# Optimization experiments

Hardware: AMD Instinct MI355X
Metric: run time of the kernel (lower is better)

Reference implementation:

```python
import jax, jax.numpy as jnp
import numpy as np

BETA_MIN = 0.1
BETA_MAX = 20.0
T_MIN = 1e-4
T_MAX = 1.0
N_ITER = 256
B, D, K = 8192, 32, 64


def setup_inputs() -> dict:
    key = jax.random.key(0)
    k1, k2, k3, k4, k5 = jax.random.split(key, 5)
    return {
        "x_init": jax.random.normal(k1, (B, D), jnp.float32),
        "centers": jax.random.normal(k2, (K, D), jnp.float32),
        # stds kept away from 0 so the t->0 mixture variances stay well conditioned
        "stds": jax.random.uniform(k3, (K, D), jnp.float32, minval=0.2, maxval=1.0),
        "weights": jax.random.uniform(k4, (K,), jnp.float32, minval=0.1, maxval=1.0),
        # Brownian increments for every Euler-Maruyama step (pre-drawn for determinism)
        "noise": jax.random.normal(k5, (N_ITER - 1, B, D), jnp.float32),
    }


def _beta(t):
    # linear beta schedule
    return BETA_MIN + (BETA_MAX - BETA_MIN) * t


def _Beta(t):
    # integral of beta
    return BETA_MIN * t + 0.5 * (BETA_MAX - BETA_MIN) * t * t


def reference(x_init, centers, stds, weights, noise):
    log_w = jnp.log(weights)  # [K]
    times = jnp.linspace(T_MIN, T_MAX, N_ITER)[::-1]  # reversed schedule

    def grad_log_prob(x, t):
        # exact Gaussian-mixture score of the VP-diffused density at time t
        eB = jnp.exp(-_Beta(t))
        m = jnp.sqrt(eB) * centers                    # [K, D] diffused means
        v = eB * stds * stds + (1.0 - eB)             # [K, D] diffused variances
        diff = x[:, None, :] - m[None, :, :]          # [B, K, D]
        # faithful to the original (including the ndim/2 * sum(log) normalization term)
        logc = (-0.5 * jnp.sum(diff * diff / v, axis=-1)
                - (0.5 * D) * jnp.sum(jnp.log(2.0 * np.pi * v), axis=-1)
                + log_w)                              # [B, K]
        r = jax.nn.softmax(logc, axis=1)              # responsibilities [B, K]
        return -jnp.einsum('bk,bkd->bd', r, diff / v) # grad_x log p_t(x)

    def step(x, inp):
        t, t_next, z = inp
        dt = t_next - t                               # negative (reverse time)
        bt = _beta(t)
        score = grad_log_prob(x, t)
        # reverse VP-SDE drift: f - g^2 * score = -0.5*beta*x - beta*score
        drift = -0.5 * bt * x - bt * score
        x = x + drift * dt + jnp.sqrt(bt) * z * jnp.sqrt(jnp.abs(dt))
        return x, None

    x, _ = jax.lax.scan(step, x_init, (times[:-1], times[1:], noise))
    return x
```

## Files before the change

### kernel.cpp

```cpp
#include <hip/hip_runtime.h>
#include <math.h>


namespace {

constexpr int BD   = 8192;
constexpr int DIMN = 32;
constexpr int KM   = 64;
constexpr int NST  = 255;
constexpr float TMINc = 1e-4f, TMAXc = 1.0f;
constexpr float BMIN = 0.1f,  BMAX = 20.0f;
constexpr float L2E = 1.4426950408889634f;
constexpr float LN2 = 0.6931471805599453f;

template <int CTRL>
__device__ __forceinline__ float dpp_addf(float v) {
  int o = __builtin_amdgcn_update_dpp(0, __float_as_int(v), CTRL, 0xf, 0xf, true);
  return v + __int_as_float(o);
}
__device__ __forceinline__ float dred8(float v) {
  v = dpp_addf<0xB1>(v);
  v = dpp_addf<0x4E>(v);
  v = dpp_addf<0x141>(v);
  return v;
}

__global__ __launch_bounds__(256, 2) void sbm_kernel(
    const float* __restrict__ xin,
    const float* __restrict__ cen_g,
    const float* __restrict__ std_g,
    const float* __restrict__ w_g,
    const float* __restrict__ noi,
    float* __restrict__ out)
{
  __shared__ __align__(16) float s_iv[2][KM][DIMN];
  __shared__ __align__(16) float s_a [2][KM][DIMN];
  __shared__ __align__(16) float s_c [2][KM];
  __shared__ __align__(16) float4 s_n [2][4][2][64];
  __shared__ float2 s_ml[2][4][2][8];

  const int tid  = threadIdx.x;
  const int w    = tid >> 6;
  const int lane = tid & 63;
  const int dc   = lane & 7;
  const int slot = lane >> 3;
  const int d0   = dc * 4;
  const int k0   = w * 16;
  const int b0   = blockIdx.x * 16 + slot;
  const int b1   = b0 + 8;

  const int gk = tid >> 2;
  const int gd = (tid & 3) * 8;

  float cen[8], s2[8];
#pragma unroll
  for (int i = 0; i < 8; ++i) {
    cen[i] = cen_g[gk * DIMN + gd + i];
    float s = std_g[gk * DIMN + gd + i];
    s2[i] = s * s;
  }
  const float lw2 = __builtin_amdgcn_logf(w_g[gk]);

  float x0[4], x1[4];
  {
    const float4 a = *reinterpret_cast<const float4*>(xin + b0 * DIMN + d0);
    const float4 b = *reinterpret_cast<const float4*>(xin + b1 * DIMN + d0);
    x0[0]=a.x; x0[1]=a.y; x0[2]=a.z; x0[3]=a.w;
    x1[0]=b.x; x1[1]=b.y; x1[2]=b.z; x1[3]=b.w;
  }

  auto gen = [&](int buf, int jj) {
    const float t  = fmaf((float)(255 - jj) * (1.0f / 255.0f), (TMAXc - TMINc), TMINc);
    const float Bt = fmaf(0.5f * (BMAX - BMIN), t * t, BMIN * t);
    const float eB  = __builtin_amdgcn_exp2f(-Bt * L2E);
    const float om  = 1.0f - eB;
    const float smB = __builtin_amdgcn_sqrtf(eB);
    float cq = 0.0f, c2 = 0.0f;
    float ivv[8], av[8];
#pragma unroll
    for (int i = 0; i < 8; ++i) {
      const float v  = fmaf(eB, s2[i], om);
      const float iv = L2E * __builtin_amdgcn_rcpf(v);
      const float m  = smB * cen[i];
      const float A  = m * iv;
      ivv[i] = iv; av[i] = A;
      cq = fmaf(m, A, cq);
      c2 += __builtin_amdgcn_logf(v);
    }
    *reinterpret_cast<float4*>(&s_iv[buf][gk][gd])     = make_float4(ivv[0], ivv[1], ivv[2], ivv[3]);
    *reinterpret_cast<float4*>(&s_iv[buf][gk][gd + 4]) = make_float4(ivv[4], ivv[5], ivv[6], ivv[7]);
    *reinterpret_cast<float4*>(&s_a [buf][gk][gd])     = make_float4(av[0], av[1], av[2], av[3]);
    *reinterpret_cast<float4*>(&s_a [buf][gk][gd + 4]) = make_float4(av[4], av[5], av[6], av[7]);
    float q1 = dpp_addf<0xB1>(cq); q1 = dpp_addf<0x4E>(q1);
    float q2 = dpp_addf<0xB1>(c2); q2 = dpp_addf<0x4E>(q2);
    if ((tid & 3) == 0)
      s_c[buf][gk] = fmaf(-16.0f, q2, fmaf(-0.5f, q1, lw2));
  };

  gen(0, 0);
  __syncthreads();

#pragma unroll 1
  for (int j = 0; j < NST; ++j) {
    const int buf = j & 1;

    const float4 z0 = *reinterpret_cast<const float4*>(
        noi + ((size_t)j * BD + b0) * (size_t)DIMN + d0);
    const float4 z1 = *reinterpret_cast<const float4*>(
        noi + ((size_t)j * BD + b1) * (size_t)DIMN + d0);

    if (j + 1 < NST) gen(buf ^ 1, j + 1);

    const float t  = fmaf((float)(255 - j) * (1.0f / 255.0f), (TMAXc - TMINc), TMINc);
    const float tn = fmaf((float)(254 - j) * (1.0f / 255.0f), (TMAXc - TMINc), TMINc);
    const float dt = tn - t;
    const float bt = fmaf(BMAX - BMIN, t, BMIN);

    float h0[4], h1[4];
#pragma unroll
    for (int i = 0; i < 4; ++i) { h0[i] = -0.5f * x0[i] * x0[i]; h1[i] = -0.5f * x1[i] * x1[i]; }

    float M0 = -__builtin_inff(), M1 = -__builtin_inff();
    float L0 = 0.0f, L1 = 0.0f;
    float SIV0[4] = {0,0,0,0}, SA0[4] = {0,0,0,0};
    float SIV1[4] = {0,0,0,0}, SA1[4] = {0,0,0,0};

#pragma unroll
    for (int c = 0; c < 2; ++c) {
      const int kc = k0 + c * 8;
      const float4 ccl = *reinterpret_cast<const float4*>(&s_c[buf][kc]);
      const float4 cch = *reinterpret_cast<const float4*>(&s_c[buf][kc + 4]);
      const float cc[8] = {ccl.x, ccl.y, ccl.z, ccl.w, cch.x, cch.y, cch.z, cch.w};

      float4 tiv[8], ta[8];
      float p0[8], p1[8];
      float cm0 = -__builtin_inff(), cm1 = -__builtin_inff();
#pragma unroll
      for (int kk = 0; kk < 8; ++kk) {
        tiv[kk] = *reinterpret_cast<const float4*>(&s_iv[buf][kc + kk][d0]);
        ta[kk]  = *reinterpret_cast<const float4*>(&s_a [buf][kc + kk][d0]);
        float pa = h0[0] * tiv[kk].x;
        pa = fmaf(x0[0], ta[kk].x, pa);
        pa = fmaf(h0[1], tiv[kk].y, pa);
        pa = fmaf(x0[1], ta[kk].y, pa);
        pa = fmaf(h0[2], tiv[kk].z, pa);
        pa = fmaf(x0[2], ta[kk].z, pa);
        pa = fmaf(h0[3], tiv[kk].w, pa);
        pa = fmaf(x0[3], ta[kk].w, pa);
        float pb = h1[0] * tiv[kk].x;
        pb = fmaf(x1[0], ta[kk].x, pb);
        pb = fmaf(h1[1], tiv[kk].y, pb);
        pb = fmaf(x1[1], ta[kk].y, pb);
        pb = fmaf(h1[2], tiv[kk].z, pb);
        pb = fmaf(x1[2], ta[kk].z, pb);
        pb = fmaf(h1[3], tiv[kk].w, pb);
        pb = fmaf(x1[3], ta[kk].w, pb);
        pa = dred8(pa) + cc[kk];
        pb = dred8(pb) + cc[kk];
        p0[kk] = pa; p1[kk] = pb;
        cm0 = fmaxf(cm0, pa); cm1 = fmaxf(cm1, pb);
      }
      const float nM0 = fmaxf(M0, cm0), nM1 = fmaxf(M1, cm1);
      const float al0 = __builtin_amdgcn_exp2f(M0 - nM0);
      const float al1 = __builtin_amdgcn_exp2f(M1 - nM1);
      M0 = nM0; M1 = nM1;
      L0 *= al0; L1 *= al1;
#pragma unroll
      for (int i = 0; i < 4; ++i) {
        SIV0[i] *= al0; SA0[i] *= al0;
        SIV1[i] *= al1; SA1[i] *= al1;
      }
#pragma unroll
      for (int kk = 0; kk < 8; ++kk) {
        const float e0 = __builtin_amdgcn_exp2f(p0[kk] - M0);
        const float e1 = __builtin_amdgcn_exp2f(p1[kk] - M1);
        L0 += e0; L1 += e1;
        SIV0[0] = fmaf(e0, tiv[kk].x, SIV0[0]);
        SIV0[1] = fmaf(e0, tiv[kk].y, SIV0[1]);
        SIV0[2] = fmaf(e0, tiv[kk].z, SIV0[2]);
        SIV0[3] = fmaf(e0, tiv[kk].w, SIV0[3]);
        SA0[0]  = fmaf(e0, ta[kk].x, SA0[0]);
        SA0[1]  = fmaf(e0, ta[kk].y, SA0[1]);
        SA0[2]  = fmaf(e0, ta[kk].z, SA0[2]);
        SA0[3]  = fmaf(e0, ta[kk].w, SA0[3]);
        SIV1[0] = fmaf(e1, tiv[kk].x, SIV1[0]);
        SIV1[1] = fmaf(e1, tiv[kk].y, SIV1[1]);
        SIV1[2] = fmaf(e1, tiv[kk].z, SIV1[2]);
        SIV1[3] = fmaf(e1, tiv[kk].w, SIV1[3]);
        SA1[0]  = fmaf(e1, ta[kk].x, SA1[0]);
        SA1[1]  = fmaf(e1, ta[kk].y, SA1[1]);
        SA1[2]  = fmaf(e1, ta[kk].z, SA1[2]);
        SA1[3]  = fmaf(e1, ta[kk].w, SA1[3]);
      }
    }

    const float4 n0 = make_float4(fmaf(-x0[0], SIV0[0], SA0[0]),
                                  fmaf(-x0[1], SIV0[1], SA0[1]),
                                  fmaf(-x0[2], SIV0[2], SA0[2]),
                                  fmaf(-x0[3], SIV0[3], SA0[3]));
    const float4 n1 = make_float4(fmaf(-x1[0], SIV1[0], SA1[0]),
                                  fmaf(-x1[1], SIV1[1], SA1[1]),
                                  fmaf(-x1[2], SIV1[2], SA1[2]),
                                  fmaf(-x1[3], SIV1[3], SA1[3]));
    s_n[buf][w][0][lane] = n0;
    s_n[buf][w][1][lane] = n1;
    if (dc == 0) {
      s_ml[buf][w][0][slot] = make_float2(M0, L0);
      s_ml[buf][w][1][slot] = make_float2(M1, L1);
    }
    __syncthreads();

    const float cA  = fmaf(-0.5f * bt, dt, 1.0f);
    const float cb0 = (-bt * dt) * LN2;
    const float sq  = __builtin_amdgcn_sqrtf(bt) * __builtin_amdgcn_sqrtf(-dt);
    const int w1 = w ^ 1, w2 = w ^ 2, w3 = w ^ 3;

    {
      const float2 mA = s_ml[buf][w1][0][slot];
      const float2 mB = s_ml[buf][w2][0][slot];
      const float2 mC = s_ml[buf][w3][0][slot];
      const float Gm = fmaxf(fmaxf(M0, mA.x), fmaxf(mB.x, mC.x));
      const float ss = __builtin_amdgcn_exp2f(M0 - Gm);
      const float sA = __builtin_amdgcn_exp2f(mA.x - Gm);
      const float sB = __builtin_amdgcn_exp2f(mB.x - Gm);
      const float sC = __builtin_amdgcn_exp2f(mC.x - Gm);
      float Lt = ss * L0;
      Lt = fmaf(sA, mA.y, Lt); Lt = fmaf(sB, mB.y, Lt); Lt = fmaf(sC, mC.y, Lt);
      const float4 nA = s_n[buf][w1][0][lane];
      const float4 nB = s_n[buf][w2][0][lane];
      const float4 nC = s_n[buf][w3][0][lane];
      float nu[4] = {ss * n0.x, ss * n0.y, ss * n0.z, ss * n0.w};
      nu[0] = fmaf(sA, nA.x, nu[0]); nu[1] = fmaf(sA, nA.y, nu[1]);
      nu[2] = fmaf(sA, nA.z, nu[2]); nu[3] = fmaf(sA, nA.w, nu[3]);
      nu[0] = fmaf(sB, nB.x, nu[0]); nu[1] = fmaf(sB, nB.y, nu[1]);
      nu[2] = fmaf(sB, nB.z, nu[2]); nu[3] = fmaf(sB, nB.w, nu[3]);
      nu[0] = fmaf(sC, nC.x, nu[0]); nu[1] = fmaf(sC, nC.y, nu[1]);
      nu[2] = fmaf(sC, nC.z, nu[2]); nu[3] = fmaf(sC, nC.w, nu[3]);
      const float cb2 = cb0 * __builtin_amdgcn_rcpf(Lt);
      const float zc[4] = {z0.x, z0.y, z0.z, z0.w};
#pragma unroll
      for (int i = 0; i < 4; ++i)
        x0[i] = fmaf(cb2, nu[i], fmaf(cA, x0[i], sq * zc[i]));
    }
    {
      const float2 mA = s_ml[buf][w1][1][slot];
      const float2 mB = s_ml[buf][w2][1][slot];
      const float2 mC = s_ml[buf][w3][1][slot];
      const float Gm = fmaxf(fmaxf(M1, mA.x), fmaxf(mB.x, mC.x));
      const float ss = __builtin_amdgcn_exp2f(M1 - Gm);
      const float sA = __builtin_amdgcn_exp2f(mA.x - Gm);
      const float sB = __builtin_amdgcn_exp2f(mB.x - Gm);
      const float sC = __builtin_amdgcn_exp2f(mC.x - Gm);
      float Lt = ss * L1;
      Lt = fmaf(sA, mA.y, Lt); Lt = fmaf(sB, mB.y, Lt); Lt = fmaf(sC, mC.y, Lt);
      const float4 nA = s_n[buf][w1][1][lane];
      const float4 nB = s_n[buf][w2][1][lane];
      const float4 nC = s_n[buf][w3][1][lane];
      float nu[4] = {ss * n1.x, ss * n1.y, ss * n1.z, ss * n1.w};
      nu[0] = fmaf(sA, nA.x, nu[0]); nu[1] = fmaf(sA, nA.y, nu[1]);
      nu[2] = fmaf(sA, nA.z, nu[2]); nu[3] = fmaf(sA, nA.w, nu[3]);
      nu[0] = fmaf(sB, nB.x, nu[0]); nu[1] = fmaf(sB, nB.y, nu[1]);
      nu[2] = fmaf(sB, nB.z, nu[2]); nu[3] = fmaf(sB, nB.w, nu[3]);
      nu[0] = fmaf(sC, nC.x, nu[0]); nu[1] = fmaf(sC, nC.y, nu[1]);
      nu[2] = fmaf(sC, nC.z, nu[2]); nu[3] = fmaf(sC, nC.w, nu[3]);
      const float cb2 = cb0 * __builtin_amdgcn_rcpf(Lt);
      const float zc[4] = {z1.x, z1.y, z1.z, z1.w};
#pragma unroll
      for (int i = 0; i < 4; ++i)
        x1[i] = fmaf(cb2, nu[i], fmaf(cA, x1[i], sq * zc[i]));
    }
  }

  if (w == 0) {
    *reinterpret_cast<float4*>(out + b0 * DIMN + d0) = make_float4(x0[0], x0[1], x0[2], x0[3]);
    *reinterpret_cast<float4*>(out + b1 * DIMN + d0) = make_float4(x1[0], x1[1], x1[2], x1[3]);
  }
}

}

extern "C" void kernel_launch(void* const* d_in, const int* in_sizes, int n_in,
                              void* d_out, int out_size, void* d_ws, size_t ws_size,
                              hipStream_t stream) {
  const float* x_init  = (const float*)d_in[0];
  const float* centers = (const float*)d_in[1];
  const float* stds    = (const float*)d_in[2];
  const float* weights = (const float*)d_in[3];
  const float* noise   = (const float*)d_in[4];
  float* out = (float*)d_out;

  sbm_kernel<<<dim3(512), dim3(256), 0, stream>>>(x_init, centers, stds, weights,
                                                  noise, out);
}
```

Before: 1.172 ms.

## Split mixture components across eight waves and merge via shared-memory x state

```diff
diff --git a/kernel.cpp b/kernel.cpp
--- a/kernel.cpp
+++ b/kernel.cpp
@@ -25,7 +25,7 @@
   return v;
 }
 
-__global__ __launch_bounds__(256, 2) void sbm_kernel(
+__global__ __launch_bounds__(512, 4) void sbm_kernel(
     const float* __restrict__ xin,
     const float* __restrict__ cen_g,
     const float* __restrict__ std_g,
@@ -33,11 +33,12 @@
     const float* __restrict__ noi,
     float* __restrict__ out)
 {
-  __shared__ __align__(16) float s_iv[2][KM][DIMN];
-  __shared__ __align__(16) float s_a [2][KM][DIMN];
-  __shared__ __align__(16) float s_c [2][KM];
-  __shared__ __align__(16) float4 s_n [2][4][2][64];
-  __shared__ float2 s_ml[2][4][2][8];
+  __shared__ __align__(16) float  s_iv[2][KM][DIMN];
+  __shared__ __align__(16) float  s_a [2][KM][DIMN];
+  __shared__ __align__(16) float  s_c [2][KM];
+  __shared__ __align__(16) float4 s_n [8][16][8];
+  __shared__ __align__(16) float2 s_ml[8][16];
+  __shared__ __align__(16) float  s_x [16][DIMN];
 
   const int tid  = threadIdx.x;
   const int w    = tid >> 6;
@@ -45,29 +46,22 @@
   const int dc   = lane & 7;
   const int slot = lane >> 3;
   const int d0   = dc * 4;
-  const int k0   = w * 16;
-  const int b0   = blockIdx.x * 16 + slot;
-  const int b1   = b0 + 8;
-
-  const int gk = tid >> 2;
-  const int gd = (tid & 3) * 8;
-
-  float cen[8], s2[8];
-#pragma unroll
-  for (int i = 0; i < 8; ++i) {
-    cen[i] = cen_g[gk * DIMN + gd + i];
-    float s = std_g[gk * DIMN + gd + i];
-    s2[i] = s * s;
+  const int k0   = w * 8;
+  const int bbase = blockIdx.x * 16;
+
+  const int gk = tid >> 3;
+  const int gd = (tid & 7) * 4;
+  float cen[4], s2[4];
+  {
+    const float4 c4 = *reinterpret_cast<const float4*>(cen_g + gk * DIMN + gd);
+    const float4 s4 = *reinterpret_cast<const float4*>(std_g + gk * DIMN + gd);
+    cen[0]=c4.x; cen[1]=c4.y; cen[2]=c4.z; cen[3]=c4.w;
+    s2[0]=s4.x*s4.x; s2[1]=s4.y*s4.y; s2[2]=s4.z*s4.z; s2[3]=s4.w*s4.w;
   }
   const float lw2 = __builtin_amdgcn_logf(w_g[gk]);
 
-  float x0[4], x1[4];
-  {
-    const float4 a = *reinterpret_cast<const float4*>(xin + b0 * DIMN + d0);
-    const float4 b = *reinterpret_cast<const float4*>(xin + b1 * DIMN + d0);
-    x0[0]=a.x; x0[1]=a.y; x0[2]=a.z; x0[3]=a.w;
-    x1[0]=b.x; x1[1]=b.y; x1[2]=b.z; x1[3]=b.w;
-  }
+  const int mb = (w << 1) + (lane >> 5);
+  const int md = lane & 31;
 
   auto gen = [&](int buf, int jj) {
     const float t  = fmaf((float)(255 - jj) * (1.0f / 255.0f), (TMAXc - TMINc), TMINc);
@@ -75,28 +69,28 @@
     const float eB  = __builtin_amdgcn_exp2f(-Bt * L2E);
     const float om  = 1.0f - eB;
     const float smB = __builtin_amdgcn_sqrtf(eB);
-    float cq = 0.0f, c2 = 0.0f;
-    float ivv[8], av[8];
-#pragma unroll
-    for (int i = 0; i < 8; ++i) {
+    float cq = 0.0f, pv = 1.0f;
+    float ivv[4], av[4];
+#pragma unroll
+    for (int i = 0; i < 4; ++i) {
       const float v  = fmaf(eB, s2[i], om);
       const float iv = L2E * __builtin_amdgcn_rcpf(v);
       const float m  = smB * cen[i];
       const float A  = m * iv;
       ivv[i] = iv; av[i] = A;
       cq = fmaf(m, A, cq);
-      c2 += __builtin_amdgcn_logf(v);
-    }
-    *reinterpret_cast<float4*>(&s_iv[buf][gk][gd])     = make_float4(ivv[0], ivv[1], ivv[2], ivv[3]);
-    *reinterpret_cast<float4*>(&s_iv[buf][gk][gd + 4]) = make_float4(ivv[4], ivv[5], ivv[6], ivv[7]);
-    *reinterpret_cast<float4*>(&s_a [buf][gk][gd])     = make_float4(av[0], av[1], av[2], av[3]);
-    *reinterpret_cast<float4*>(&s_a [buf][gk][gd + 4]) = make_float4(av[4], av[5], av[6], av[7]);
-    float q1 = dpp_addf<0xB1>(cq); q1 = dpp_addf<0x4E>(q1);
-    float q2 = dpp_addf<0xB1>(c2); q2 = dpp_addf<0x4E>(q2);
-    if ((tid & 3) == 0)
+      pv *= v;
+    }
+    *reinterpret_cast<float4*>(&s_iv[buf][gk][gd]) = make_float4(ivv[0], ivv[1], ivv[2], ivv[3]);
+    *reinterpret_cast<float4*>(&s_a [buf][gk][gd]) = make_float4(av[0], av[1], av[2], av[3]);
+    const float q1 = dred8(cq);
+    const float q2 = dred8(__builtin_amdgcn_logf(pv));
+    if ((tid & 7) == 0)
       s_c[buf][gk] = fmaf(-16.0f, q2, fmaf(-0.5f, q1, lw2));
   };
 
+  float x_m = xin[(size_t)(bbase + mb) * DIMN + md];
+  s_x[mb][md] = x_m;
   gen(0, 0);
   __syncthreads();
 
@@ -104,10 +98,15 @@
   for (int j = 0; j < NST; ++j) {
     const int buf = j & 1;
 
-    const float4 z0 = *reinterpret_cast<const float4*>(
-        noi + ((size_t)j * BD + b0) * (size_t)DIMN + d0);
-    const float4 z1 = *reinterpret_cast<const float4*>(
-        noi + ((size_t)j * BD + b1) * (size_t)DIMN + d0);
+    const float z_m = noi[((size_t)j * BD + (bbase + mb)) * (size_t)DIMN + md];
+
+    float x0[4], x1[4];
+    {
+      const float4 a = *reinterpret_cast<const float4*>(&s_x[slot][d0]);
+      const float4 b = *reinterpret_cast<const float4*>(&s_x[slot + 8][d0]);
+      x0[0]=a.x; x0[1]=a.y; x0[2]=a.z; x0[3]=a.w;
+      x1[0]=b.x; x1[1]=b.y; x1[2]=b.z; x1[3]=b.w;
+    }
 
     if (j + 1 < NST) gen(buf ^ 1, j + 1);
 
@@ -120,23 +119,22 @@
 #pragma unroll
     for (int i = 0; i < 4; ++i) { h0[i] = -0.5f * x0[i] * x0[i]; h1[i] = -0.5f * x1[i] * x1[i]; }
 
-    float M0 = -__builtin_inff(), M1 = -__builtin_inff();
+    float M0 = 0.0f, M1 = 0.0f;
     float L0 = 0.0f, L1 = 0.0f;
     float SIV0[4] = {0,0,0,0}, SA0[4] = {0,0,0,0};
     float SIV1[4] = {0,0,0,0}, SA1[4] = {0,0,0,0};
 
 #pragma unroll
-    for (int c = 0; c < 2; ++c) {
-      const int kc = k0 + c * 8;
-      const float4 ccl = *reinterpret_cast<const float4*>(&s_c[buf][kc]);
-      const float4 cch = *reinterpret_cast<const float4*>(&s_c[buf][kc + 4]);
-      const float cc[8] = {ccl.x, ccl.y, ccl.z, ccl.w, cch.x, cch.y, cch.z, cch.w};
-
-      float4 tiv[8], ta[8];
-      float p0[8], p1[8];
+    for (int sc = 0; sc < 2; ++sc) {
+      const int kc = k0 + sc * 4;
+      const float4 ccv = *reinterpret_cast<const float4*>(&s_c[buf][kc]);
+      const float cc[4] = {ccv.x, ccv.y, ccv.z, ccv.w};
+
+      float4 tiv[4], ta[4];
+      float p0[4], p1[4];
       float cm0 = -__builtin_inff(), cm1 = -__builtin_inff();
 #pragma unroll
-      for (int kk = 0; kk < 8; ++kk) {
+      for (int kk = 0; kk < 4; ++kk) {
         tiv[kk] = *reinterpret_cast<const float4*>(&s_iv[buf][kc + kk][d0]);
         ta[kk]  = *reinterpret_cast<const float4*>(&s_a [buf][kc + kk][d0]);
         float pa = h0[0] * tiv[kk].x;
@@ -160,18 +158,22 @@
         p0[kk] = pa; p1[kk] = pb;
         cm0 = fmaxf(cm0, pa); cm1 = fmaxf(cm1, pb);
       }
-      const float nM0 = fmaxf(M0, cm0), nM1 = fmaxf(M1, cm1);
-      const float al0 = __builtin_amdgcn_exp2f(M0 - nM0);
-      const float al1 = __builtin_amdgcn_exp2f(M1 - nM1);
-      M0 = nM0; M1 = nM1;
-      L0 *= al0; L1 *= al1;
-#pragma unroll
-      for (int i = 0; i < 4; ++i) {
-        SIV0[i] *= al0; SA0[i] *= al0;
-        SIV1[i] *= al1; SA1[i] *= al1;
-      }
-#pragma unroll
-      for (int kk = 0; kk < 8; ++kk) {
+      if (sc == 0) {
+        M0 = cm0; M1 = cm1;
+      } else {
+        const float nM0 = fmaxf(M0, cm0), nM1 = fmaxf(M1, cm1);
+        const float al0 = __builtin_amdgcn_exp2f(M0 - nM0);
+        const float al1 = __builtin_amdgcn_exp2f(M1 - nM1);
+        M0 = nM0; M1 = nM1;
+        L0 *= al0; L1 *= al1;
+#pragma unroll
+        for (int i = 0; i < 4; ++i) {
+          SIV0[i] *= al0; SA0[i] *= al0;
+          SIV1[i] *= al1; SA1[i] *= al1;
+        }
+      }
+#pragma unroll
+      for (int kk = 0; kk < 4; ++kk) {
         const float e0 = __builtin_amdgcn_exp2f(p0[kk] - M0);
         const float e1 = __builtin_amdgcn_exp2f(p1[kk] - M1);
         L0 += e0; L1 += e1;
@@ -194,86 +196,51 @@
       }
     }
 
-    const float4 n0 = make_float4(fmaf(-x0[0], SIV0[0], SA0[0]),
-                                  fmaf(-x0[1], SIV0[1], SA0[1]),
-                                  fmaf(-x0[2], SIV0[2], SA0[2]),
-                                  fmaf(-x0[3], SIV0[3], SA0[3]));
-    const float4 n1 = make_float4(fmaf(-x1[0], SIV1[0], SA1[0]),
-                                  fmaf(-x1[1], SIV1[1], SA1[1]),
-                                  fmaf(-x1[2], SIV1[2], SA1[2]),
-                                  fmaf(-x1[3], SIV1[3], SA1[3]));
-    s_n[buf][w][0][lane] = n0;
-    s_n[buf][w][1][lane] = n1;
-    if (dc == 0) {
-      s_ml[buf][w][0][slot] = make_float2(M0, L0);
-      s_ml[buf][w][1][slot] = make_float2(M1, L1);
+    {
+      const float4 n0 = make_float4(fmaf(-x0[0], SIV0[0], SA0[0]),
+                                    fmaf(-x0[1], SIV0[1], SA0[1]),
+                                    fmaf(-x0[2], SIV0[2], SA0[2]),
+                                    fmaf(-x0[3], SIV0[3], SA0[3]));
+      const float4 n1 = make_float4(fmaf(-x1[0], SIV1[0], SA1[0]),
+                                    fmaf(-x1[1], SIV1[1], SA1[1]),
+                                    fmaf(-x1[2], SIV1[2], SA1[2]),
+                                    fmaf(-x1[3], SIV1[3], SA1[3]));
+      s_n[w][slot][dc]     = n0;
+      s_n[w][slot + 8][dc] = n1;
+      if (dc == 0) {
+        s_ml[w][slot]     = make_float2(M0, L0);
+        s_ml[w][slot + 8] = make_float2(M1, L1);
+      }
     }
     __syncthreads();
 
-    const float cA  = fmaf(-0.5f * bt, dt, 1.0f);
-    const float cb0 = (-bt * dt) * LN2;
-    const float sq  = __builtin_amdgcn_sqrtf(bt) * __builtin_amdgcn_sqrtf(-dt);
-    const int w1 = w ^ 1, w2 = w ^ 2, w3 = w ^ 3;
-
     {
-      const float2 mA = s_ml[buf][w1][0][slot];
-      const float2 mB = s_ml[buf][w2][0][slot];
-      const float2 mC = s_ml[buf][w3][0][slot];
-      const float Gm = fmaxf(fmaxf(M0, mA.x), fmaxf(mB.x, mC.x));
-      const float ss = __builtin_amdgcn_exp2f(M0 - Gm);
-      const float sA = __builtin_amdgcn_exp2f(mA.x - Gm);
-      const float sB = __builtin_amdgcn_exp2f(mB.x - Gm);
-      const float sC = __builtin_amdgcn_exp2f(mC.x - Gm);
-      float Lt = ss * L0;
-      Lt = fmaf(sA, mA.y, Lt); Lt = fmaf(sB, mB.y, Lt); Lt = fmaf(sC, mC.y, Lt);
-      const float4 nA = s_n[buf][w1][0][lane];
-      const float4 nB = s_n[buf][w2][0][lane];
-      const float4 nC = s_n[buf][w3][0][lane];
-      float nu[4] = {ss * n0.x, ss * n0.y, ss * n0.z, ss * n0.w};
-      nu[0] = fmaf(sA, nA.x, nu[0]); nu[1] = fmaf(sA, nA.y, nu[1]);
-      nu[2] = fmaf(sA, nA.z, nu[2]); nu[3] = fmaf(sA, nA.w, nu[3]);
-      nu[0] = fmaf(sB, nB.x, nu[0]); nu[1] = fmaf(sB, nB.y, nu[1]);
-      nu[2] = fmaf(sB, nB.z, nu[2]); nu[3] = fmaf(sB, nB.w, nu[3]);
-      nu[0] = fmaf(sC, nC.x, nu[0]); nu[1] = fmaf(sC, nC.y, nu[1]);
-      nu[2] = fmaf(sC, nC.z, nu[2]); nu[3] = fmaf(sC, nC.w, nu[3]);
+      const float cA  = fmaf(-0.5f * bt, dt, 1.0f);
+      const float cb0 = (-bt * dt) * LN2;
+      const float sq  = __builtin_amdgcn_sqrtf(bt) * __builtin_amdgcn_sqrtf(-dt);
+
+      float Mv[8], Lv[8];
+#pragma unroll
+      for (int q = 0; q < 8; ++q) {
+        const float2 ml = s_ml[q][mb];
+        Mv[q] = ml.x; Lv[q] = ml.y;
+      }
+      const float Gm = fmaxf(fmaxf(fmaxf(Mv[0], Mv[1]), fmaxf(Mv[2], Mv[3])),
+                             fmaxf(fmaxf(Mv[4], Mv[5]), fmaxf(Mv[6], Mv[7])));
+      float Lt = 0.0f, nu = 0.0f;
+#pragma unroll
+      for (int q = 0; q < 8; ++q) {
+        const float s = __builtin_amdgcn_exp2f(Mv[q] - Gm);
+        Lt = fmaf(s, Lv[q], Lt);
+        nu = fmaf(s, reinterpret_cast<const float*>(&s_n[q][mb][0])[md], nu);
+      }
       const float cb2 = cb0 * __builtin_amdgcn_rcpf(Lt);
-      const float zc[4] = {z0.x, z0.y, z0.z, z0.w};
-#pragma unroll
-      for (int i = 0; i < 4; ++i)
-        x0[i] = fmaf(cb2, nu[i], fmaf(cA, x0[i], sq * zc[i]));
-    }
-    {
-      const float2 mA = s_ml[buf][w1][1][slot];
-      const float2 mB = s_ml[buf][w2][1][slot];
-      const float2 mC = s_ml[buf][w3][1][slot];
-      const float Gm = fmaxf(fmaxf(M1, mA.x), fmaxf(mB.x, mC.x));
-      const float ss = __builtin_amdgcn_exp2f(M1 - Gm);
-      const float sA = __builtin_amdgcn_exp2f(mA.x - Gm);
-      const float sB = __builtin_amdgcn_exp2f(mB.x - Gm);
-      const float sC = __builtin_amdgcn_exp2f(mC.x - Gm);
-      float Lt = ss * L1;
-      Lt = fmaf(sA, mA.y, Lt); Lt = fmaf(sB, mB.y, Lt); Lt = fmaf(sC, mC.y, Lt);
-      const float4 nA = s_n[buf][w1][1][lane];
-      const float4 nB = s_n[buf][w2][1][lane];
-      const float4 nC = s_n[buf][w3][1][lane];
-      float nu[4] = {ss * n1.x, ss * n1.y, ss * n1.z, ss * n1.w};
-      nu[0] = fmaf(sA, nA.x, nu[0]); nu[1] = fmaf(sA, nA.y, nu[1]);
-      nu[2] = fmaf(sA, nA.z, nu[2]); nu[3] = fmaf(sA, nA.w, nu[3]);
-      nu[0] = fmaf(sB, nB.x, nu[0]); nu[1] = fmaf(sB, nB.y, nu[1]);
-      nu[2] = fmaf(sB, nB.z, nu[2]); nu[3] = fmaf(sB, nB.w, nu[3]);
-      nu[0] = fmaf(sC, nC.x, nu[0]); nu[1] = fmaf(sC, nC.y, nu[1]);
-      nu[2] = fmaf(sC, nC.z, nu[2]); nu[3] = fmaf(sC, nC.w, nu[3]);
-      const float cb2 = cb0 * __builtin_amdgcn_rcpf(Lt);
-      const float zc[4] = {z1.x, z1.y, z1.z, z1.w};
-#pragma unroll
-      for (int i = 0; i < 4; ++i)
-        x1[i] = fmaf(cb2, nu[i], fmaf(cA, x1[i], sq * zc[i]));
-    }
-  }
-
-  if (w == 0) {
-    *reinterpret_cast<float4*>(out + b0 * DIMN + d0) = make_float4(x0[0], x0[1], x0[2], x0[3]);
-    *reinterpret_cast<float4*>(out + b1 * DIMN + d0) = make_float4(x1[0], x1[1], x1[2], x1[3]);
+      const float xn  = fmaf(cb2, nu, fmaf(cA, x_m, sq * z_m));
+      s_x[mb][md] = xn;
+      if (j == NST - 1) out[(size_t)(bbase + mb) * DIMN + md] = xn;
+      x_m = xn;
+    }
+    __syncthreads();
   }
 }
 
@@ -289,6 +256,6 @@
   const float* noise   = (const float*)d_in[4];
   float* out = (float*)d_out;
 
-  sbm_kernel<<<dim3(512), dim3(256), 0, stream>>>(x_init, centers, stds, weights,
+  sbm_kernel<<<dim3(512), dim3(512), 0, stream>>>(x_init, centers, stds, weights,
                                                   noise, out);
 }
```

New measurement: 1.217 ms. 1.04x slower.
